# Optimization experiments

Hardware: AMD Instinct MI355X
Metric: run time of the kernel (lower is better)

## Reference

```python
import jax, jax.numpy as jnp
import numpy as np

def setup_inputs() -> dict:
    key = jax.random.key(0)
    k0, k1, k2, k3 = jax.random.split(key, 4)
    B, L, D, E, Dg = 2, 2048, 2048, 8, 256  # Dg = D // E
    x = jax.random.normal(k0, (B, L, D), dtype=jnp.float32)
    Wg = jax.random.normal(k1, (E, D), dtype=jnp.float32) * 0.02     # gate: Linear(D, E)
    Wd = jax.random.normal(k2, (E, Dg, D), dtype=jnp.float32) * 0.02  # down: Linear(D, Dg) per expert
    Wu = jax.random.normal(k3, (E, D, Dg), dtype=jnp.float32) * 0.02  # up:   Linear(Dg, D) per expert
    return {"x": x, "Wg": Wg, "Wd": Wd, "Wu": Wu, "k": 2}

def reference(x, Wg, Wd, Wu, k):
    B, L, D = x.shape
    E = Wg.shape[0]
    T = B * L
    xf = x.reshape(T, D)
    # gate scores: sigmoid(x @ Wg^T), then top-k gate values G and expert indices I
    S = jax.nn.sigmoid(xf @ Wg.T)            # [T, E]
    G, I = jax.lax.top_k(S, k)               # [T, k], [T, k]
    # combine weights per token per expert (zero for unselected experts);
    # equivalent to the original's one_hot + per-expert gather/scatter-add.
    w = jnp.zeros((T, E), x.dtype).at[jnp.arange(T)[:, None], I].add(G)  # [T, E]
    # down: sum_e w[t,e] * (Wd[e] @ x[t])
    down = jnp.einsum('te,egd,td->tg', w, Wd, xf)   # [T, Dg]
    # inner model is identity
    # up: sum_e w[t,e] * (Wu[e] @ down[t])
    up = jnp.einsum('te,edg,tg->td', w, Wu, down)   # [T, D]
    return up.reshape(B, L, D)
```

## Files before the change

### kernel.cpp

```cpp
#include <hip/hip_runtime.h>
#include <hip/hip_bf16.h>
#include <stdint.h>

#define T_TOK 4096
#define DIM   2048
#define NEXP  8
#define DG    256
#define TOPK  2

#define BM 64
#define BN 128
#define BK 32
#define NROWS  (T_TOK*TOPK + NEXP*BM)
#define NBLK_M (NROWS/BM)

typedef __attribute__((ext_vector_type(8))) short short8;
typedef __attribute__((ext_vector_type(4))) float f32x4;

static __device__ __forceinline__ short f2bf(float f) {
    union { float f; uint32_t u; } v{f};
    uint32_t r = v.u + 0x7fffu + ((v.u >> 16) & 1u);
    return (short)(r >> 16);
}
static __device__ __forceinline__ float b2f(short s) {
    union { uint32_t u; float f; } v{((uint32_t)(unsigned short)s) << 16};
    return v.f;
}

#define GLD16(g, l) \
    __builtin_amdgcn_global_load_lds((const __attribute__((address_space(1))) void*)(g), \
                                     (__attribute__((address_space(3))) void*)(l), 16, 0, 0)

__global__ __launch_bounds__(256) void gate_kernel(const float* __restrict__ x,
                                                   const float* __restrict__ Wg,
                                                   int* __restrict__ gidx,
                                                   float* __restrict__ gval,
                                                   short* __restrict__ x_bf)
{
    int token = blockIdx.x * 4 + (threadIdx.x >> 6);
    int lane  = threadIdx.x & 63;
    const float4* xr = (const float4*)(x + (size_t)token * DIM);

    float4 xv[8];
#pragma unroll
    for (int i = 0; i < 8; i++) xv[i] = xr[lane + 64 * i];

    short4* xb = (short4*)(x_bf + (size_t)token * DIM);
#pragma unroll
    for (int i = 0; i < 8; i++) {
        short4 o;
        o.x = f2bf(xv[i].x); o.y = f2bf(xv[i].y);
        o.z = f2bf(xv[i].z); o.w = f2bf(xv[i].w);
        xb[lane + 64 * i] = o;
    }

    float acc[NEXP];
#pragma unroll
    for (int e = 0; e < NEXP; e++) {
        const float4* wr = (const float4*)(Wg + e * DIM);
        float a = 0.0f;
#pragma unroll
        for (int i = 0; i < 8; i++) {
            float4 w = wr[lane + 64 * i];
            a += xv[i].x * w.x + xv[i].y * w.y + xv[i].z * w.z + xv[i].w * w.w;
        }
        acc[e] = a;
    }

#pragma unroll
    for (int m = 1; m < 64; m <<= 1) {
#pragma unroll
        for (int e = 0; e < NEXP; e++) acc[e] += __shfl_xor(acc[e], m, 64);
    }

    if (lane == 0) {
        float sg[NEXP];
#pragma unroll
        for (int e = 0; e < NEXP; e++) sg[e] = 1.0f / (1.0f + expf(-acc[e]));
        int i0 = 0;
#pragma unroll
        for (int e = 1; e < NEXP; e++) if (sg[e] > sg[i0]) i0 = e;
        int i1 = (i0 == 0) ? 1 : 0;
#pragma unroll
        for (int e = 0; e < NEXP; e++) if (e != i0 && e != i1 && sg[e] > sg[i1]) i1 = e;
        gidx[2 * token + 0] = i0;
        gidx[2 * token + 1] = i1;
        gval[2 * token + 0] = sg[i0];
        gval[2 * token + 1] = sg[i1];
    }
}

__global__ __launch_bounds__(256) void convW_kernel(const float* __restrict__ Wd,
                                                    const float* __restrict__ Wu,
                                                    short* __restrict__ Wd_bf,
                                                    short* __restrict__ Wu_bf,
                                                    int n4)
{
    int i = blockIdx.x * 256 + threadIdx.x;
    const float* s; short* d; int j;
    if (i < n4)      { s = Wd; d = Wd_bf; j = i; }
    else             { s = Wu; d = Wu_bf; j = i - n4; if (j >= n4) return; }
    float4 v = ((const float4*)s)[j];
    short4 o;
    o.x = f2bf(v.x); o.y = f2bf(v.y); o.z = f2bf(v.z); o.w = f2bf(v.w);
    ((short4*)d)[j] = o;
}

__global__ __launch_bounds__(1024) void bucket_kernel(const int* __restrict__ gidx,
                                                      int* __restrict__ rowtok,
                                                      int* __restrict__ rowpos,
                                                      int* __restrict__ seg_off)
{
    __shared__ int cnt[NEXP];
    __shared__ int cur[NEXP];
    int tid = threadIdx.x;
    if (tid < NEXP) cnt[tid] = 0;
    __syncthreads();

    for (int t = tid; t < T_TOK; t += 1024) {
        atomicAdd(&cnt[gidx[2 * t + 0]], 1);
        atomicAdd(&cnt[gidx[2 * t + 1]], 1);
    }
    __syncthreads();

    if (tid == 0) {
        int o = 0;
        for (int e = 0; e < NEXP; e++) {
            seg_off[e] = o;
            cur[e] = o;
            o += ((cnt[e] + BM - 1) / BM) * BM;
        }
        seg_off[NEXP] = o;
    }
    __syncthreads();

    for (int r = tid; r < NROWS; r += 1024) rowtok[r] = -1;
    __syncthreads();

    for (int t = tid; t < T_TOK; t += 1024) {
        for (int s = 0; s < TOPK; s++) {
            int e = gidx[2 * t + s];
            int p = atomicAdd(&cur[e], 1);
            rowtok[p] = t;
            rowpos[2 * t + s] = p;
        }
    }
}

template<int K, int Ntot>
__global__ __launch_bounds__(256) void gemm_kernel(const short* __restrict__ A,
                                                   const short* __restrict__ B,
                                                   const int* __restrict__ rowtok,
                                                   const int* __restrict__ seg_off,
                                                   short* __restrict__ C)
{
    __shared__ short As[BM][BK];
    __shared__ short Bs[BN][BK];

    int row0 = blockIdx.x * BM;
    int total = seg_off[NEXP];
    if (row0 >= total) return;
    int e = 0;
    while (row0 >= seg_off[e + 1]) ++e;
    int n0 = blockIdx.y * BN;

    int tid = threadIdx.x;
    int w = tid >> 6, l = tid & 63;

    int ar = (w << 4) + (l >> 2);
    int achunk = (l & 3) ^ ((l >> 3) & 3);
    int ta = rowtok[row0 + ar]; if (ta < 0) ta = 0;
    const short* ag  = A + (size_t)ta * K + achunk * 8;

    const short* be  = B + (size_t)e * Ntot * K + (size_t)n0 * K;
    const short* bg0 = be + (size_t)(((w * 2 + 0) << 4) + (l >> 2)) * K + achunk * 8;
    const short* bg1 = be + (size_t)(((w * 2 + 1) << 4) + (l >> 2)) * K + achunk * 8;

    auto ldsA  = (__attribute__((address_space(3))) void*)&As[w << 4][0];
    auto ldsB0 = (__attribute__((address_space(3))) void*)&Bs[(w * 2 + 0) << 4][0];
    auto ldsB1 = (__attribute__((address_space(3))) void*)&Bs[(w * 2 + 1) << 4][0];

    int mlane = l & 15, qlane = l >> 4;
    int rchunk = ((qlane ^ ((l >> 1) & 3)) << 3);
    int wm = w >> 1, wn = w & 1;
    const short* pA0 = &As[wm * 32 + mlane][rchunk];
    const short* pA1 = pA0 + 16 * BK;
    const short* pB0 = &Bs[wn * 64 + mlane][rchunk];
    const short* pB1 = pB0 + 16 * BK;
    const short* pB2 = pB0 + 32 * BK;
    const short* pB3 = pB0 + 48 * BK;

    f32x4 acc[2][4] = {};

    for (int k0 = 0; k0 < K; k0 += BK) {
        GLD16(ag, ldsA);
        GLD16(bg0, ldsB0);
        GLD16(bg1, ldsB1);
        ag += BK; bg0 += BK; bg1 += BK;
        __syncthreads();

        short8 a0 = *(const short8*)pA0;
        short8 a1 = *(const short8*)pA1;
        short8 b0 = *(const short8*)pB0;
        short8 b1 = *(const short8*)pB1;
        short8 b2 = *(const short8*)pB2;
        short8 b3 = *(const short8*)pB3;

        acc[0][0] = __builtin_amdgcn_mfma_f32_16x16x32_bf16(a0, b0, acc[0][0], 0, 0, 0);
        acc[0][1] = __builtin_amdgcn_mfma_f32_16x16x32_bf16(a0, b1, acc[0][1], 0, 0, 0);
        acc[0][2] = __builtin_amdgcn_mfma_f32_16x16x32_bf16(a0, b2, acc[0][2], 0, 0, 0);
        acc[0][3] = __builtin_amdgcn_mfma_f32_16x16x32_bf16(a0, b3, acc[0][3], 0, 0, 0);
        acc[1][0] = __builtin_amdgcn_mfma_f32_16x16x32_bf16(a1, b0, acc[1][0], 0, 0, 0);
        acc[1][1] = __builtin_amdgcn_mfma_f32_16x16x32_bf16(a1, b1, acc[1][1], 0, 0, 0);
        acc[1][2] = __builtin_amdgcn_mfma_f32_16x16x32_bf16(a1, b2, acc[1][2], 0, 0, 0);
        acc[1][3] = __builtin_amdgcn_mfma_f32_16x16x32_bf16(a1, b3, acc[1][3], 0, 0, 0);
        __syncthreads();
    }

#pragma unroll
    for (int i = 0; i < 2; i++) {
        int rbase = row0 + wm * 32 + i * 16 + qlane * 4;
#pragma unroll
        for (int j = 0; j < 4; j++) {
            int col = n0 + wn * 64 + j * 16 + mlane;
#pragma unroll
            for (int r = 0; r < 4; r++)
                C[(size_t)(rbase + r) * Ntot + col] = f2bf(acc[i][j][r]);
        }
    }
}

__global__ __launch_bounds__(256) void combine1_kernel(const short* __restrict__ dr,
                                                       const int* __restrict__ rowpos,
                                                       const float* __restrict__ gval,
                                                       short* __restrict__ dt)
{
    int t = blockIdx.x, d = threadIdx.x;
    int   p0 = rowpos[2 * t], p1 = rowpos[2 * t + 1];
    float g0 = gval[2 * t],   g1 = gval[2 * t + 1];
    float v = g0 * b2f(dr[(size_t)p0 * DG + d]) + g1 * b2f(dr[(size_t)p1 * DG + d]);
    dt[(size_t)t * DG + d] = f2bf(v);
}

__global__ __launch_bounds__(256) void combine2_kernel(const short* __restrict__ ur,
                                                       const int* __restrict__ rowpos,
                                                       const float* __restrict__ gval,
                                                       float* __restrict__ out)
{
    int i = blockIdx.x * 256 + threadIdx.x;
    int t = i >> 9;
    int c = (i & 511) * 4;
    int   p0 = rowpos[2 * t], p1 = rowpos[2 * t + 1];
    float g0 = gval[2 * t],   g1 = gval[2 * t + 1];
    short4 u0 = *(const short4*)&ur[(size_t)p0 * DIM + c];
    short4 u1 = *(const short4*)&ur[(size_t)p1 * DIM + c];
    float4 o;
    o.x = g0 * b2f(u0.x) + g1 * b2f(u1.x);
    o.y = g0 * b2f(u0.y) + g1 * b2f(u1.y);
    o.z = g0 * b2f(u0.z) + g1 * b2f(u1.z);
    o.w = g0 * b2f(u0.w) + g1 * b2f(u1.w);
    *(float4*)&out[(size_t)t * DIM + c] = o;
}

extern "C" void kernel_launch(void* const* d_in, const int* in_sizes, int n_in,
                              void* d_out, int out_size, void* d_ws, size_t ws_size,
                              hipStream_t stream) {
    const float* x  = (const float*)d_in[0];
    const float* Wg = (const float*)d_in[1];
    const float* Wd = (const float*)d_in[2];
    const float* Wu = (const float*)d_in[3];
    float* out = (float*)d_out;

    char* p = (char*)d_ws;
    int*   gidx    = (int*)(p + 0);
    float* gval    = (float*)(p + 32768);
    int*   rowtok  = (int*)(p + 65536);
    int*   rowpos  = (int*)(p + 100352);
    int*   seg_off = (int*)(p + 133120);
    short* x_bf    = (short*)(p + 133376);
    short* Wd_bf   = (short*)(p + 133376 + 16777216);
    short* Wu_bf   = Wd_bf + 4194304;
    short* dr_bf   = Wu_bf + 4194304;
    short* dt_bf   = dr_bf + (size_t)NROWS * DG;
    short* ur_bf   = dt_bf + (size_t)T_TOK * DG;

    const int W4 = NEXP * DG * DIM / 4;
    gate_kernel<<<T_TOK / 4, 256, 0, stream>>>(x, Wg, gidx, gval, x_bf);
    convW_kernel<<<(2 * W4 + 255) / 256, 256, 0, stream>>>(Wd, Wu, Wd_bf, Wu_bf, W4);
    bucket_kernel<<<1, 1024, 0, stream>>>(gidx, rowtok, rowpos, seg_off);

    gemm_kernel<DIM, DG><<<dim3(NBLK_M, DG / BN), 256, 0, stream>>>(x_bf, Wd_bf, rowtok, seg_off, dr_bf);
    combine1_kernel<<<T_TOK, 256, 0, stream>>>(dr_bf, rowpos, gval, dt_bf);
    gemm_kernel<DG, DIM><<<dim3(NBLK_M, DIM / BN), 256, 0, stream>>>(dt_bf, Wu_bf, rowtok, seg_off, ur_bf);
    combine2_kernel<<<T_TOK * DIM / 4 / 256, 256, 0, stream>>>(ur_bf, rowpos, gval, out);
}
```

Baseline: 200.1 us.

## Double-buffer LDS tiles and widen K step to 64 in expert GEMM

Restructures the grouped expert GEMM to use two LDS buffers with a K tile of 64, issuing async global-to-LDS loads for the next tile while MFMAs run on the current one. This halves the number of barrier-separated iterations and overlaps memory latency with compute. The XOR swizzle is widened to 8 chunks to match the 64-wide rows. In exchange LDS use per block rises to about 48KB, which can lower occupancy.

Result: no change. 197.0 us, median of 2 (-1.5%).

```diff
diff --git a/kernel.cpp b/kernel.cpp
--- a/kernel.cpp
+++ b/kernel.cpp
@@ -1,5 +1,4 @@
 #include <hip/hip_runtime.h>
-#include <hip/hip_bf16.h>
 #include <stdint.h>
 
 #define T_TOK 4096
@@ -10,7 +9,7 @@
 
 #define BM 64
 #define BN 128
-#define BK 32
+#define BKU 64
 #define NROWS  (T_TOK*TOPK + NEXP*BM)
 #define NBLK_M (NROWS/BM)
 
@@ -147,6 +146,50 @@
     }
 }
 
+#define AS3 __attribute__((address_space(3)))
+
+#define STAGE(B_) do { \
+    GLD16(agA0, lA_##B_##_0); \
+    GLD16(agA1, lA_##B_##_1); \
+    GLD16(agB0, lB_##B_##_0); \
+    GLD16(agB1, lB_##B_##_1); \
+    GLD16(agB2, lB_##B_##_2); \
+    GLD16(agB3, lB_##B_##_3); \
+    agA0 += BKU; agA1 += BKU; \
+    agB0 += BKU; agB1 += BKU; agB2 += BKU; agB3 += BKU; \
+} while (0)
+
+#define COMP(B_) do { \
+    short8 a00 = *(const short8*)&As[B_][am0][c0]; \
+    short8 a10 = *(const short8*)&As[B_][am1][c0]; \
+    short8 b00 = *(const short8*)&Bs[B_][bn0][c0]; \
+    short8 b10 = *(const short8*)&Bs[B_][bn1][c0]; \
+    short8 b20 = *(const short8*)&Bs[B_][bn2][c0]; \
+    short8 b30 = *(const short8*)&Bs[B_][bn3][c0]; \
+    short8 a01 = *(const short8*)&As[B_][am0][c1]; \
+    short8 a11 = *(const short8*)&As[B_][am1][c1]; \
+    short8 b01 = *(const short8*)&Bs[B_][bn0][c1]; \
+    short8 b11 = *(const short8*)&Bs[B_][bn1][c1]; \
+    short8 b21 = *(const short8*)&Bs[B_][bn2][c1]; \
+    short8 b31 = *(const short8*)&Bs[B_][bn3][c1]; \
+    acc[0][0] = __builtin_amdgcn_mfma_f32_16x16x32_bf16(a00, b00, acc[0][0], 0, 0, 0); \
+    acc[0][1] = __builtin_amdgcn_mfma_f32_16x16x32_bf16(a00, b10, acc[0][1], 0, 0, 0); \
+    acc[0][2] = __builtin_amdgcn_mfma_f32_16x16x32_bf16(a00, b20, acc[0][2], 0, 0, 0); \
+    acc[0][3] = __builtin_amdgcn_mfma_f32_16x16x32_bf16(a00, b30, acc[0][3], 0, 0, 0); \
+    acc[1][0] = __builtin_amdgcn_mfma_f32_16x16x32_bf16(a10, b00, acc[1][0], 0, 0, 0); \
+    acc[1][1] = __builtin_amdgcn_mfma_f32_16x16x32_bf16(a10, b10, acc[1][1], 0, 0, 0); \
+    acc[1][2] = __builtin_amdgcn_mfma_f32_16x16x32_bf16(a10, b20, acc[1][2], 0, 0, 0); \
+    acc[1][3] = __builtin_amdgcn_mfma_f32_16x16x32_bf16(a10, b30, acc[1][3], 0, 0, 0); \
+    acc[0][0] = __builtin_amdgcn_mfma_f32_16x16x32_bf16(a01, b01, acc[0][0], 0, 0, 0); \
+    acc[0][1] = __builtin_amdgcn_mfma_f32_16x16x32_bf16(a01, b11, acc[0][1], 0, 0, 0); \
+    acc[0][2] = __builtin_amdgcn_mfma_f32_16x16x32_bf16(a01, b21, acc[0][2], 0, 0, 0); \
+    acc[0][3] = __builtin_amdgcn_mfma_f32_16x16x32_bf16(a01, b31, acc[0][3], 0, 0, 0); \
+    acc[1][0] = __builtin_amdgcn_mfma_f32_16x16x32_bf16(a11, b01, acc[1][0], 0, 0, 0); \
+    acc[1][1] = __builtin_amdgcn_mfma_f32_16x16x32_bf16(a11, b11, acc[1][1], 0, 0, 0); \
+    acc[1][2] = __builtin_amdgcn_mfma_f32_16x16x32_bf16(a11, b21, acc[1][2], 0, 0, 0); \
+    acc[1][3] = __builtin_amdgcn_mfma_f32_16x16x32_bf16(a11, b31, acc[1][3], 0, 0, 0); \
+} while (0)
+
 template<int K, int Ntot>
 __global__ __launch_bounds__(256) void gemm_kernel(const short* __restrict__ A,
                                                    const short* __restrict__ B,
@@ -154,8 +197,8 @@
                                                    const int* __restrict__ seg_off,
                                                    short* __restrict__ C)
 {
-    __shared__ short As[BM][BK];
-    __shared__ short Bs[BN][BK];
+    __shared__ __align__(16) short As[2][BM][BKU];
+    __shared__ __align__(16) short Bs[2][BN][BKU];
 
     int row0 = blockIdx.x * BM;
     int total = seg_off[NEXP];
@@ -167,53 +210,51 @@
     int tid = threadIdx.x;
     int w = tid >> 6, l = tid & 63;
 
-    int ar = (w << 4) + (l >> 2);
-    int achunk = (l & 3) ^ ((l >> 3) & 3);
-    int ta = rowtok[row0 + ar]; if (ta < 0) ta = 0;
-    const short* ag  = A + (size_t)ta * K + achunk * 8;
-
-    const short* be  = B + (size_t)e * Ntot * K + (size_t)n0 * K;
-    const short* bg0 = be + (size_t)(((w * 2 + 0) << 4) + (l >> 2)) * K + achunk * 8;
-    const short* bg1 = be + (size_t)(((w * 2 + 1) << 4) + (l >> 2)) * K + achunk * 8;
-
-    auto ldsA  = (__attribute__((address_space(3))) void*)&As[w << 4][0];
-    auto ldsB0 = (__attribute__((address_space(3))) void*)&Bs[(w * 2 + 0) << 4][0];
-    auto ldsB1 = (__attribute__((address_space(3))) void*)&Bs[(w * 2 + 1) << 4][0];
+    int srow = (w << 3) + (l >> 3);
+    int sc   = ((l & 7) ^ ((l >> 3) & 7)) << 3;
+
+    int ta0 = rowtok[row0 + srow];      if (ta0 < 0) ta0 = 0;
+    int ta1 = rowtok[row0 + 32 + srow]; if (ta1 < 0) ta1 = 0;
+    const short* agA0 = A + (size_t)ta0 * K + sc;
+    const short* agA1 = A + (size_t)ta1 * K + sc;
+    const short* be = B + (size_t)e * Ntot * K + (size_t)n0 * K;
+    const short* agB0 = be + (size_t)(srow     ) * K + sc;
+    const short* agB1 = be + (size_t)(srow + 32) * K + sc;
+    const short* agB2 = be + (size_t)(srow + 64) * K + sc;
+    const short* agB3 = be + (size_t)(srow + 96) * K + sc;
+
+    auto lA_0_0 = (AS3 void*)&As[0][(w << 3)     ][0];
+    auto lA_0_1 = (AS3 void*)&As[0][(w << 3) + 32][0];
+    auto lA_1_0 = (AS3 void*)&As[1][(w << 3)     ][0];
+    auto lA_1_1 = (AS3 void*)&As[1][(w << 3) + 32][0];
+    auto lB_0_0 = (AS3 void*)&Bs[0][(w << 3)     ][0];
+    auto lB_0_1 = (AS3 void*)&Bs[0][(w << 3) + 32][0];
+    auto lB_0_2 = (AS3 void*)&Bs[0][(w << 3) + 64][0];
+    auto lB_0_3 = (AS3 void*)&Bs[0][(w << 3) + 96][0];
+    auto lB_1_0 = (AS3 void*)&Bs[1][(w << 3)     ][0];
+    auto lB_1_1 = (AS3 void*)&Bs[1][(w << 3) + 32][0];
+    auto lB_1_2 = (AS3 void*)&Bs[1][(w << 3) + 64][0];
+    auto lB_1_3 = (AS3 void*)&Bs[1][(w << 3) + 96][0];
 
     int mlane = l & 15, qlane = l >> 4;
-    int rchunk = ((qlane ^ ((l >> 1) & 3)) << 3);
     int wm = w >> 1, wn = w & 1;
-    const short* pA0 = &As[wm * 32 + mlane][rchunk];
-    const short* pA1 = pA0 + 16 * BK;
-    const short* pB0 = &Bs[wn * 64 + mlane][rchunk];
-    const short* pB1 = pB0 + 16 * BK;
-    const short* pB2 = pB0 + 32 * BK;
-    const short* pB3 = pB0 + 48 * BK;
+    int c0 = (qlane ^ (mlane & 7)) << 3;
+    int c1 = c0 ^ 32;
+    int am0 = wm * 32 + mlane, am1 = am0 + 16;
+    int bn0 = wn * 64 + mlane, bn1 = bn0 + 16, bn2 = bn0 + 32, bn3 = bn0 + 48;
 
     f32x4 acc[2][4] = {};
 
-    for (int k0 = 0; k0 < K; k0 += BK) {
-        GLD16(ag, ldsA);
-        GLD16(bg0, ldsB0);
-        GLD16(bg1, ldsB1);
-        ag += BK; bg0 += BK; bg1 += BK;
+    STAGE(0);
+    __syncthreads();
+    constexpr int NT = K / BKU;
+#pragma unroll 1
+    for (int t = 0; t < NT; t += 2) {
+        if (t + 1 < NT) STAGE(1);
+        COMP(0);
         __syncthreads();
-
-        short8 a0 = *(const short8*)pA0;
-        short8 a1 = *(const short8*)pA1;
-        short8 b0 = *(const short8*)pB0;
-        short8 b1 = *(const short8*)pB1;
-        short8 b2 = *(const short8*)pB2;
-        short8 b3 = *(const short8*)pB3;
-
-        acc[0][0] = __builtin_amdgcn_mfma_f32_16x16x32_bf16(a0, b0, acc[0][0], 0, 0, 0);
-        acc[0][1] = __builtin_amdgcn_mfma_f32_16x16x32_bf16(a0, b1, acc[0][1], 0, 0, 0);
-        acc[0][2] = __builtin_amdgcn_mfma_f32_16x16x32_bf16(a0, b2, acc[0][2], 0, 0, 0);
-        acc[0][3] = __builtin_amdgcn_mfma_f32_16x16x32_bf16(a0, b3, acc[0][3], 0, 0, 0);
-        acc[1][0] = __builtin_amdgcn_mfma_f32_16x16x32_bf16(a1, b0, acc[1][0], 0, 0, 0);
-        acc[1][1] = __builtin_amdgcn_mfma_f32_16x16x32_bf16(a1, b1, acc[1][1], 0, 0, 0);
-        acc[1][2] = __builtin_amdgcn_mfma_f32_16x16x32_bf16(a1, b2, acc[1][2], 0, 0, 0);
-        acc[1][3] = __builtin_amdgcn_mfma_f32_16x16x32_bf16(a1, b3, acc[1][3], 0, 0, 0);
+        if (t + 2 < NT) STAGE(0);
+        COMP(1);
         __syncthreads();
     }
 
@@ -229,6 +270,10 @@
         }
     }
 }
+
+#undef STAGE
+#undef COMP
+#undef AS3
 
 __global__ __launch_bounds__(256) void combine1_kernel(const short* __restrict__ dr,
                                                        const int* __restrict__ rowpos,
```
